# Optimization experiments

Measured on AMD Instinct MI355X. Metric: run time of the kernel, lower is better.

Reference implementation:

```python
import jax, jax.numpy as jnp
import numpy as np

HEADS = 16
S = 1024      # affine_dim
B, L = 4, 2048


def _conv1x1(x, W, b):
    # Conv1d with kernel_size=1: pointwise channel mixing. x: (B, C, L)
    return jnp.einsum('oc,bcl->bol', W, x) + b[None, :, None]


def setup_inputs() -> dict:
    key = jax.random.key(0)
    ks = jax.random.split(key, 7)
    scale = 1.0 / np.sqrt(S)  # ~ torch Conv1d default init scale
    return {
        'x':  jax.random.normal(ks[0], (B, S, L), dtype=jnp.float32),
        'Wk': jax.random.normal(ks[1], (S, S), dtype=jnp.float32) * scale,
        'bk': jax.random.normal(ks[2], (S,), dtype=jnp.float32) * scale,
        'Wq': jax.random.normal(ks[3], (S, S), dtype=jnp.float32) * scale,
        'bq': jax.random.normal(ks[4], (S,), dtype=jnp.float32) * scale,
        'Wp': jax.random.normal(ks[5], (S, S), dtype=jnp.float32) * scale,
        'bp': jax.random.normal(ks[6], (S,), dtype=jnp.float32) * scale,
    }


def reference(x, Wk, bk, Wq, bq, Wp, bp):
    b, c, l = x.shape
    h = HEADS
    d = c // h
    keys = _conv1x1(x, Wk, bk).reshape(b, h, d, l)
    queries = _conv1x1(x, Wq, bq).reshape(b, h, d, l)
    # scores[b,h,i,j] = sum_d keys[...,d,i] * queries[...,d,j]  (keys^T @ queries)
    # NOTE: original scales by `seqlen ** 1 / 2` == seqlen / 2 (Python precedence),
    # i.e. multiply by 2/L, NOT 1/sqrt(L). Faithfully preserved.
    scores = jnp.einsum('bhdi,bhdj->bhij', keys, queries) * (2.0 / l)
    attn = jax.nn.softmax(scores, axis=-1)
    xh = x.reshape(b, h, d, l)  # raw x used as values
    out = jnp.einsum('bhdi,bhij->bhdj', xh, attn).reshape(b, c, l)
    return _conv1x1(out, Wp, bp)
```

## Files before the change

kernel.cpp:

```cpp
#include <hip/hip_runtime.h>
#include <hip/hip_bf16.h>
#include <cstdint>
#include <cstddef>

#ifndef __has_builtin
#define __has_builtin(x) 0
#endif

#define DEVI __device__ __forceinline__

typedef __attribute__((ext_vector_type(8))) __bf16 bf16x8;
typedef __attribute__((ext_vector_type(4))) float float4v;
typedef __attribute__((ext_vector_type(16))) float float16v;
typedef __attribute__((ext_vector_type(4))) unsigned short ushort4v;
typedef __attribute__((ext_vector_type(4))) unsigned int uint4v;

constexpr int Bd = 4, Sd = 1024, Ld = 2048, Hd = 16, Dd = 64;

DEVI unsigned short f2bf(float x){
  union { float f; unsigned u; } v; v.f = x;
  unsigned r = v.u + 0x7fffu + ((v.u >> 16) & 1u);
  return (unsigned short)(r >> 16);
}

DEVI unsigned pack2(float lo, float hi){
  union { float f; unsigned u; } a, b; a.f = lo; b.f = hi;
  unsigned ra = a.u + 0x7fffu + ((a.u >> 16) & 1u);
  unsigned rb = b.u + 0x7fffu + ((b.u >> 16) & 1u);
#if __has_builtin(__builtin_amdgcn_perm)
  return __builtin_amdgcn_perm(rb, ra, 0x07060302u);
#else
  return (ra >> 16) | (rb & 0xffff0000u);
#endif
}

DEVI float fast_exp2(float x){
#if __has_builtin(__builtin_amdgcn_exp2f)
  return __builtin_amdgcn_exp2f(x);
#else
  return exp2f(x);
#endif
}

DEVI void plane32_swap(unsigned &a, unsigned &b){
  asm("v_permlane32_swap_b32 %0, %1" : "+v"(a), "+v"(b));
}

DEVI void gload_lds16(const void* g, void* lds){
  __builtin_amdgcn_global_load_lds(
      (const __attribute__((address_space(1))) void*)g,
      (__attribute__((address_space(3))) void*)lds,
      16, 0, 0);
}

DEVI float4v mfma_bf16(bf16x8 a, bf16x8 b, float4v c){
  return __builtin_amdgcn_mfma_f32_16x16x32_bf16(a, b, c, 0, 0, 0);
}

DEVI float16v mfma32_bf16(bf16x8 a, bf16x8 b, float16v c){
  return __builtin_amdgcn_mfma_f32_32x32x16_bf16(a, b, c, 0, 0, 0);
}


__global__ void wcast_kernel(const float* __restrict__ Wk, const float* __restrict__ Wq,
                             const float* __restrict__ Wp,
                             unsigned short* __restrict__ Wkbf, unsigned short* __restrict__ Wqbf,
                             unsigned short* __restrict__ Wpbf, float ck){
  size_t i = ((size_t)blockIdx.x * 256 + threadIdx.x) * 4;
  float4v a = *(const float4v*)(Wk + i);
  float4v b = *(const float4v*)(Wq + i);
  float4v c = *(const float4v*)(Wp + i);
  ushort4v oa = { f2bf(a[0]*ck), f2bf(a[1]*ck), f2bf(a[2]*ck), f2bf(a[3]*ck) };
  ushort4v ob = { f2bf(b[0]), f2bf(b[1]), f2bf(b[2]), f2bf(b[3]) };
  ushort4v oc = { f2bf(c[0]), f2bf(c[1]), f2bf(c[2]), f2bf(c[3]) };
  *(ushort4v*)(Wkbf + i) = oa;
  *(ushort4v*)(Wqbf + i) = ob;
  *(ushort4v*)(Wpbf + i) = oc;
}

__global__ void transpose_cast(const float* __restrict__ x, unsigned short* __restrict__ Xt){
  __shared__ float tile[32][33];
  const int b = blockIdx.z;
  const int l0 = blockIdx.x * 32;
  const int s0 = blockIdx.y * 32;
  const int tx = threadIdx.x, ty = threadIdx.y;
  #pragma unroll
  for (int r = 0; r < 32; r += 8)
    tile[ty + r][tx] = x[((size_t)b*Sd + s0 + ty + r)*Ld + l0 + tx];
  __syncthreads();
  #pragma unroll
  for (int r = 0; r < 32; r += 8)
    Xt[((size_t)b*Ld + l0 + ty + r)*Sd + s0 + tx] = f2bf(tile[tx][ty + r]);
}

__global__ void vprime_kernel(const float* __restrict__ x, const float* __restrict__ invZ,
                              unsigned short* __restrict__ Vp){
  size_t idx = ((size_t)blockIdx.x * 256 + threadIdx.x) * 4;
  const int l = (int)(idx & (Ld - 1));
  const int c = (int)((idx >> 11) & (Sd - 1));
  const int b = (int)(idx >> 21);
  const int h = c >> 6;
  float4v xv = *(const float4v*)(x + idx);
  float4v zv = *(const float4v*)(invZ + ((size_t)(b*Hd + h) * Ld + l));
  ushort4v o = { f2bf(xv[0]*zv[0]), f2bf(xv[1]*zv[1]), f2bf(xv[2]*zv[2]), f2bf(xv[3]*zv[3]) };
  *(ushort4v*)(Vp + idx) = o;
}

template<int OUT_MODE>
__global__ __launch_bounds__(256, 2)
void conv_gemm(const unsigned short* __restrict__ A,
               const unsigned short* __restrict__ Bt,
               const float* __restrict__ bias, float bscale,
               unsigned short* __restrict__ outT,
               float* __restrict__ outF)
{
  constexpr int BK = 32;
  constexpr int NKSTEP = Sd / BK;
  __shared__ __attribute__((aligned(16))) unsigned short Abuf[2][128*BK];
  __shared__ __attribute__((aligned(16))) unsigned short Bbuf[2][128*BK];

  const int b  = blockIdx.z;
  const int n0 = blockIdx.x * 128;
  const int m0 = blockIdx.y * 128;
  const int tid = threadIdx.x;
  const int w = tid >> 6, lane = tid & 63, lr = lane & 15, lg = lane >> 4;
  const int wm = (w >> 1) * 64, wn = (w & 1) * 64;

  const unsigned short* Abase = A + (size_t)m0 * Sd;
  const unsigned short* Bbase = Bt + ((size_t)b * Ld + n0) * Sd;

  auto stage = [&](int bf, int kt){
    #pragma unroll
    for (int p = 0; p < 2; ++p){
      int slot = p*256 + tid;
      int row = slot >> 2, c = slot & 3;
      int csrc = c ^ ((row >> 1) & 3);
      gload_lds16(Abase + (size_t)row * Sd + kt*BK + csrc*8,
                  (void*)(&Abuf[bf][(size_t)(p*256 + w*64) * 8]));
    }
    #pragma unroll
    for (int p = 0; p < 2; ++p){
      int slot = p*256 + tid;
      int row = slot >> 2, c = slot & 3;
      int csrc = c ^ ((row >> 1) & 3);
      gload_lds16(Bbase + (size_t)row * Sd + kt*BK + csrc*8,
                  (void*)(&Bbuf[bf][(size_t)(p*256 + w*64) * 8]));
    }
  };

  const int gsw = lg ^ ((lr >> 1) & 3);

  float4v acc[4][4];
  #pragma unroll
  for (int i = 0; i < 4; ++i)
    #pragma unroll
    for (int j = 0; j < 4; ++j)
      acc[i][j] = (float4v){0.f, 0.f, 0.f, 0.f};

  stage(0, 0);
  __syncthreads();
  int cur = 0;
  for (int kt = 0; kt < NKSTEP; ++kt){
    if (kt + 1 < NKSTEP) stage(cur ^ 1, kt + 1);
    bf16x8 af[4], bfv[4];
    #pragma unroll
    for (int i = 0; i < 4; ++i){
      int row = wm + i*16 + lr;
      af[i] = *(const bf16x8*)((const char*)&Abuf[cur][0] + (size_t)row*64 + gsw*16);
    }
    #pragma unroll
    for (int j = 0; j < 4; ++j){
      int row = wn + j*16 + lr;
      bfv[j] = *(const bf16x8*)((const char*)&Bbuf[cur][0] + (size_t)row*64 + gsw*16);
    }
    #pragma unroll
    for (int i = 0; i < 4; ++i)
      #pragma unroll
      for (int j = 0; j < 4; ++j)
        acc[i][j] = mfma_bf16(af[i], bfv[j], acc[i][j]);
    __syncthreads();
    cur ^= 1;
  }

  #pragma unroll
  for (int i = 0; i < 4; ++i){
    const int mb = m0 + wm + i*16 + lg*4;
    float4v bv = *(const float4v*)(bias + mb);
    #pragma unroll
    for (int j = 0; j < 4; ++j){
      const int n = n0 + wn + j*16 + lr;
      float4v v = acc[i][j];
      float o0 = v[0] + bscale*bv[0];
      float o1 = v[1] + bscale*bv[1];
      float o2 = v[2] + bscale*bv[2];
      float o3 = v[3] + bscale*bv[3];
      if (OUT_MODE == 0){
        ushort4v o = { f2bf(o0), f2bf(o1), f2bf(o2), f2bf(o3) };
        *(ushort4v*)(outT + ((size_t)b*Ld + n)*Sd + mb) = o;
      } else {
        outF[((size_t)b*Sd + mb + 0)*Ld + n] = o0;
        outF[((size_t)b*Sd + mb + 1)*Ld + n] = o1;
        outF[((size_t)b*Sd + mb + 2)*Ld + n] = o2;
        outF[((size_t)b*Sd + mb + 3)*Ld + n] = o3;
      }
    }
  }
}

__global__ __launch_bounds__(256, 4)
void stats_kernel(const unsigned short* __restrict__ Kt,
                  const unsigned short* __restrict__ Qt,
                  float* __restrict__ invZ)
{
  __shared__ __attribute__((aligned(16))) unsigned short Qbuf[2][64*64];

  const int m = blockIdx.x;
  const int xcd = m & 7, slot = m >> 3;
  const int bh = xcd * 8 + (slot >> 4);
  const int ib = slot & 15;
  const int b = bh >> 4, h = bh & 15;
  const int i0 = ib * 128;

  const int tid = threadIdx.x, w = tid >> 6, lane = tid & 63;
  const int l31 = lane & 31, lh = lane >> 5;
  const int iw = i0 + w * 32;

  bf16x8 kb[4];
  #pragma unroll
  for (int ks = 0; ks < 4; ++ks)
    kb[ks] = *(const bf16x8*)(Kt + ((size_t)b*Ld + iw + l31)*Sd + h*64 + ks*16 + lh*8);

  const size_t qbase = (size_t)b*Ld*Sd + (size_t)h*64;
  auto stage = [&](int bf, int jt){
    const int j0 = jt * 64;
    #pragma unroll
    for (int p = 0; p < 2; ++p){
      const int slot2 = p*256 + tid;
      const int row = slot2 >> 3;
      const int gsrc = (slot2 & 7) ^ (row & 7);
      gload_lds16(Qt + qbase + (size_t)(j0 + row)*Sd + gsrc*8,
                  (void*)(&Qbuf[bf][(size_t)slot2 * 8]));
    }
  };

  float z = 0.f;
  stage(0, 0);
  __syncthreads();
  int cur = 0;
  for (int jt = 0; jt < 32; ++jt){
    if (jt + 1 < 32) stage(cur ^ 1, jt + 1);
    #pragma unroll
    for (int js = 0; js < 2; ++js){
      float16v sacc;
      #pragma unroll
      for (int r = 0; r < 16; ++r) sacc[r] = 0.f;
      #pragma unroll
      for (int ks = 0; ks < 4; ++ks){
        const int row = js*32 + l31;
        const int g = (2*ks + lh) ^ (l31 & 7);
        bf16x8 qf = *(const bf16x8*)((const char*)&Qbuf[cur][0] + (size_t)row*128 + g*16);
        sacc = mfma32_bf16(qf, kb[ks], sacc);
      }
      #pragma unroll
      for (int r = 0; r < 16; ++r) z += fast_exp2(sacc[r]);
    }
    __syncthreads();
    cur ^= 1;
  }

  z += __shfl_xor(z, 32, 64);
  if (lh == 0)
    invZ[(size_t)bh * Ld + iw + l31] = 1.0f / z;
}

__global__ __launch_bounds__(256, 4)
void attn_pv_kernel(const unsigned short* __restrict__ Kt,
                    const unsigned short* __restrict__ Qt,
                    const unsigned short* __restrict__ Vp,
                    unsigned short* __restrict__ AOt)
{
  __shared__ __attribute__((aligned(16))) unsigned short Kbuf[2][64*64];
  __shared__ __attribute__((aligned(16))) unsigned short Vbuf[2][64*64];

  const int m = blockIdx.x;
  const int xcd = m & 7, slot = m >> 3;
  const int bh = xcd * 8 + (slot >> 4);
  const int jb = slot & 15;
  const int b = bh >> 4, h = bh & 15;
  const int j0 = jb * 128;

  const int tid = threadIdx.x, w = tid >> 6, lane = tid & 63;
  const int l31 = lane & 31, lh = lane >> 5;
  const int jw = j0 + w * 32;

  bf16x8 qb[4];
  #pragma unroll
  for (int ks = 0; ks < 4; ++ks)
    qb[ks] = *(const bf16x8*)(Qt + ((size_t)b*Ld + jw + l31)*Sd + h*64 + ks*16 + lh*8);

  float16v oacc[2];
  #pragma unroll
  for (int ds = 0; ds < 2; ++ds)
    #pragma unroll
    for (int r = 0; r < 16; ++r) oacc[ds][r] = 0.f;

  const size_t kbase = (size_t)b*Ld*Sd + (size_t)h*64;
  const size_t vbase = ((size_t)b*Sd + h*64)*Ld;

  auto stage = [&](int bf, int it){
    const int i0 = it * 64;
    #pragma unroll
    for (int p = 0; p < 2; ++p){
      const int slot2 = p*256 + tid;
      const int row = slot2 >> 3;
      const int gsrc = (slot2 & 7) ^ (row & 7);
      gload_lds16(Kt + kbase + (size_t)(i0 + row)*Sd + gsrc*8,
                  (void*)(&Kbuf[bf][(size_t)slot2 * 8]));
      gload_lds16(Vp + vbase + (size_t)row*Ld + i0 + gsrc*8,
                  (void*)(&Vbuf[bf][(size_t)slot2 * 8]));
    }
  };

  stage(0, 0);
  __syncthreads();
  int cur = 0;
  for (int it = 0; it < 32; ++it){
    if (it + 1 < 32) stage(cur ^ 1, it + 1);

    float16v sacc[2];
    #pragma unroll
    for (int is = 0; is < 2; ++is){
      #pragma unroll
      for (int r = 0; r < 16; ++r) sacc[is][r] = 0.f;
      #pragma unroll
      for (int ks = 0; ks < 4; ++ks){
        const int row = is*32 + l31;
        const int g = (2*ks + lh) ^ (l31 & 7);
        bf16x8 kf = *(const bf16x8*)((const char*)&Kbuf[cur][0] + (size_t)row*128 + g*16);
        sacc[is] = mfma32_bf16(kf, qb[ks], sacc[is]);
      }
    }

    bf16x8 pf[4];
    #pragma unroll
    for (int is = 0; is < 2; ++is){
      #pragma unroll
      for (int hs = 0; hs < 2; ++hs){
        const int r0 = 8*hs;
        unsigned W0 = pack2(fast_exp2(sacc[is][r0+0]), fast_exp2(sacc[is][r0+1]));
        unsigned W1 = pack2(fast_exp2(sacc[is][r0+2]), fast_exp2(sacc[is][r0+3]));
        unsigned W2 = pack2(fast_exp2(sacc[is][r0+4]), fast_exp2(sacc[is][r0+5]));
        unsigned W3 = pack2(fast_exp2(sacc[is][r0+6]), fast_exp2(sacc[is][r0+7]));
        plane32_swap(W0, W2);
        plane32_swap(W1, W3);
        union { uint4v u; bf16x8 v; } cvt;
        cvt.u = (uint4v){ W0, W1, W2, W3 };
        pf[is*2 + hs] = cvt.v;
      }
    }

    #pragma unroll
    for (int kp = 0; kp < 4; ++kp){
      #pragma unroll
      for (int ds = 0; ds < 2; ++ds){
        const int row = ds*32 + l31;
        const int g = (2*kp + lh) ^ (l31 & 7);
        bf16x8 vf = *(const bf16x8*)((const char*)&Vbuf[cur][0] + (size_t)row*128 + g*16);
        oacc[ds] = mfma32_bf16(vf, pf[kp], oacc[ds]);
      }
    }

    __syncthreads();
    cur ^= 1;
  }

  #pragma unroll
  for (int ds = 0; ds < 2; ++ds){
    #pragma unroll
    for (int rq = 0; rq < 4; ++rq){
      const int d0 = ds*32 + 8*rq + 4*lh;
      ushort4v o = { f2bf(oacc[ds][4*rq+0]), f2bf(oacc[ds][4*rq+1]),
                     f2bf(oacc[ds][4*rq+2]), f2bf(oacc[ds][4*rq+3]) };
      *(ushort4v*)(AOt + ((size_t)b*Ld + jw + l31)*Sd + h*64 + d0) = o;
    }
  }
}


extern "C" void kernel_launch(void* const* d_in, const int* in_sizes, int n_in,
                              void* d_out, int out_size, void* d_ws, size_t ws_size,
                              hipStream_t stream)
{
  const float* x  = (const float*)d_in[0];
  const float* Wk = (const float*)d_in[1];
  const float* bk = (const float*)d_in[2];
  const float* Wq = (const float*)d_in[3];
  const float* bq = (const float*)d_in[4];
  const float* Wp = (const float*)d_in[5];
  const float* bp = (const float*)d_in[6];
  float* out = (float*)d_out;

  char* ws = (char*)d_ws;
  const size_t SZ_BLS = (size_t)Bd * Ld * Sd * 2;
  unsigned short* Xt   = (unsigned short*)(ws);
  unsigned short* Kt   = (unsigned short*)(ws + SZ_BLS);
  unsigned short* Qt   = (unsigned short*)(ws + 2*SZ_BLS);
  unsigned short* AOt  = (unsigned short*)(ws + 3*SZ_BLS);
  unsigned short* Wkbf = (unsigned short*)(ws + 4*SZ_BLS);
  unsigned short* Wqbf = (unsigned short*)(ws + 4*SZ_BLS + (size_t)2097152);
  unsigned short* Wpbf = (unsigned short*)(ws + 4*SZ_BLS + (size_t)2*2097152);
  float* invZ          = (float*)(ws + 4*SZ_BLS + (size_t)3*2097152);
  unsigned short* Vp   = Xt;

  const float ck = (2.0f / (float)Ld) * 1.44269504088896f;

  wcast_kernel<<<1024, 256, 0, stream>>>(Wk, Wq, Wp, Wkbf, Wqbf, Wpbf, ck);
  transpose_cast<<<dim3(Ld/32, Sd/32, Bd), dim3(32, 8), 0, stream>>>(x, Xt);

  dim3 cg(Ld/128, Sd/128, Bd);
  conv_gemm<0><<<cg, 256, 0, stream>>>(Wkbf, Xt, bk, ck,   Kt, nullptr);
  conv_gemm<0><<<cg, 256, 0, stream>>>(Wqbf, Xt, bq, 1.0f, Qt, nullptr);

  stats_kernel<<<dim3((Ld/128)*(Bd*Hd)), 256, 0, stream>>>(Kt, Qt, invZ);
  vprime_kernel<<<(Bd*(size_t)Sd*Ld/4)/256, 256, 0, stream>>>(x, invZ, Vp);
  attn_pv_kernel<<<dim3((Ld/128)*(Bd*Hd)), 256, 0, stream>>>(Kt, Qt, Vp, AOt);

  conv_gemm<1><<<cg, 256, 0, stream>>>(Wpbf, AOt, bp, 1.0f, nullptr, out);
}
```

Before: 235.6 us.

## Double per-wave tile in stats and attention kernels, add MFMA priority hints

Each wave in the stats and attn_pv kernels now owns 64 rows or columns instead of 32, so each LDS-staged K/Q/V tile is reused across two MFMA sub-tiles and the grid is halved. K and V fragments are loaded into registers once per iteration, and s_setprio brackets the MFMA runs. The P-to-bf16 pack switches from round-to-nearest-even to a simpler round-half-up add. The larger tiles raise register use, so launch bounds for attn_pv drop to 2 blocks per CU, trading occupancy for reuse. The grid shrinks to 512 blocks.

```diff
diff --git a/kernel.cpp b/kernel.cpp
--- a/kernel.cpp
+++ b/kernel.cpp
@@ -25,8 +25,8 @@
 
 DEVI unsigned pack2(float lo, float hi){
   union { float f; unsigned u; } a, b; a.f = lo; b.f = hi;
-  unsigned ra = a.u + 0x7fffu + ((a.u >> 16) & 1u);
-  unsigned rb = b.u + 0x7fffu + ((b.u >> 16) & 1u);
+  unsigned ra = a.u + 0x8000u;
+  unsigned rb = b.u + 0x8000u;
 #if __has_builtin(__builtin_amdgcn_perm)
   return __builtin_amdgcn_perm(rb, ra, 0x07060302u);
 #else
@@ -216,19 +216,21 @@
 
   const int m = blockIdx.x;
   const int xcd = m & 7, slot = m >> 3;
-  const int bh = xcd * 8 + (slot >> 4);
-  const int ib = slot & 15;
+  const int bh = xcd * 8 + (slot >> 3);
+  const int ib = slot & 7;
   const int b = bh >> 4, h = bh & 15;
-  const int i0 = ib * 128;
+  const int i0 = ib * 256;
 
   const int tid = threadIdx.x, w = tid >> 6, lane = tid & 63;
   const int l31 = lane & 31, lh = lane >> 5;
-  const int iw = i0 + w * 32;
-
-  bf16x8 kb[4];
-  #pragma unroll
-  for (int ks = 0; ks < 4; ++ks)
-    kb[ks] = *(const bf16x8*)(Kt + ((size_t)b*Ld + iw + l31)*Sd + h*64 + ks*16 + lh*8);
+  const int iw0 = i0 + w * 64;
+
+  bf16x8 kb[2][4];
+  #pragma unroll
+  for (int is = 0; is < 2; ++is)
+    #pragma unroll
+    for (int ks = 0; ks < 4; ++ks)
+      kb[is][ks] = *(const bf16x8*)(Kt + ((size_t)b*Ld + iw0 + is*32 + l31)*Sd + h*64 + ks*16 + lh*8);
 
   const size_t qbase = (size_t)b*Ld*Sd + (size_t)h*64;
   auto stage = [&](int bf, int jt){
@@ -243,7 +245,7 @@
     }
   };
 
-  float z = 0.f;
+  float z[2] = {0.f, 0.f};
   stage(0, 0);
   __syncthreads();
   int cur = 0;
@@ -251,29 +253,40 @@
     if (jt + 1 < 32) stage(cur ^ 1, jt + 1);
     #pragma unroll
     for (int js = 0; js < 2; ++js){
-      float16v sacc;
-      #pragma unroll
-      for (int r = 0; r < 16; ++r) sacc[r] = 0.f;
+      bf16x8 qf[4];
       #pragma unroll
       for (int ks = 0; ks < 4; ++ks){
         const int row = js*32 + l31;
         const int g = (2*ks + lh) ^ (l31 & 7);
-        bf16x8 qf = *(const bf16x8*)((const char*)&Qbuf[cur][0] + (size_t)row*128 + g*16);
-        sacc = mfma32_bf16(qf, kb[ks], sacc);
-      }
-      #pragma unroll
-      for (int r = 0; r < 16; ++r) z += fast_exp2(sacc[r]);
+        qf[ks] = *(const bf16x8*)((const char*)&Qbuf[cur][0] + (size_t)row*128 + g*16);
+      }
+      #pragma unroll
+      for (int is = 0; is < 2; ++is){
+        float16v sacc;
+        #pragma unroll
+        for (int r = 0; r < 16; ++r) sacc[r] = 0.f;
+        __builtin_amdgcn_s_setprio(1);
+        #pragma unroll
+        for (int ks = 0; ks < 4; ++ks)
+          sacc = mfma32_bf16(qf[ks], kb[is][ks], sacc);
+        __builtin_amdgcn_s_setprio(0);
+        #pragma unroll
+        for (int r = 0; r < 16; ++r) z[is] += fast_exp2(sacc[r]);
+      }
     }
     __syncthreads();
     cur ^= 1;
   }
 
-  z += __shfl_xor(z, 32, 64);
-  if (lh == 0)
-    invZ[(size_t)bh * Ld + iw + l31] = 1.0f / z;
-}
-
-__global__ __launch_bounds__(256, 4)
+  #pragma unroll
+  for (int is = 0; is < 2; ++is){
+    float zv = z[is] + __shfl_xor(z[is], 32, 64);
+    if (lh == 0)
+      invZ[(size_t)bh * Ld + iw0 + is*32 + l31] = 1.0f / zv;
+  }
+}
+
+__global__ __launch_bounds__(256, 2)
 void attn_pv_kernel(const unsigned short* __restrict__ Kt,
                     const unsigned short* __restrict__ Qt,
                     const unsigned short* __restrict__ Vp,
@@ -284,25 +297,29 @@
 
   const int m = blockIdx.x;
   const int xcd = m & 7, slot = m >> 3;
-  const int bh = xcd * 8 + (slot >> 4);
-  const int jb = slot & 15;
+  const int bh = xcd * 8 + (slot >> 3);
+  const int jb = slot & 7;
   const int b = bh >> 4, h = bh & 15;
-  const int j0 = jb * 128;
+  const int j0 = jb * 256;
 
   const int tid = threadIdx.x, w = tid >> 6, lane = tid & 63;
   const int l31 = lane & 31, lh = lane >> 5;
-  const int jw = j0 + w * 32;
-
-  bf16x8 qb[4];
-  #pragma unroll
-  for (int ks = 0; ks < 4; ++ks)
-    qb[ks] = *(const bf16x8*)(Qt + ((size_t)b*Ld + jw + l31)*Sd + h*64 + ks*16 + lh*8);
-
-  float16v oacc[2];
+  const int jw = j0 + w * 64;
+
+  bf16x8 qb[2][4];
+  #pragma unroll
+  for (int js = 0; js < 2; ++js)
+    #pragma unroll
+    for (int ks = 0; ks < 4; ++ks)
+      qb[js][ks] = *(const bf16x8*)(Qt + ((size_t)b*Ld + jw + js*32 + l31)*Sd + h*64 + ks*16 + lh*8);
+
+  float16v oacc[2][2];
   #pragma unroll
   for (int ds = 0; ds < 2; ++ds)
     #pragma unroll
-    for (int r = 0; r < 16; ++r) oacc[ds][r] = 0.f;
+    for (int js = 0; js < 2; ++js)
+      #pragma unroll
+      for (int r = 0; r < 16; ++r) oacc[ds][js][r] = 0.f;
 
   const size_t kbase = (size_t)b*Ld*Sd + (size_t)h*64;
   const size_t vbase = ((size_t)b*Sd + h*64)*Ld;
@@ -327,47 +344,58 @@
   for (int it = 0; it < 32; ++it){
     if (it + 1 < 32) stage(cur ^ 1, it + 1);
 
-    float16v sacc[2];
-    #pragma unroll
-    for (int is = 0; is < 2; ++is){
-      #pragma unroll
-      for (int r = 0; r < 16; ++r) sacc[is][r] = 0.f;
+    bf16x8 kf[2][4], vf[2][4];
+    #pragma unroll
+    for (int is = 0; is < 2; ++is)
       #pragma unroll
       for (int ks = 0; ks < 4; ++ks){
         const int row = is*32 + l31;
         const int g = (2*ks + lh) ^ (l31 & 7);
-        bf16x8 kf = *(const bf16x8*)((const char*)&Kbuf[cur][0] + (size_t)row*128 + g*16);
-        sacc[is] = mfma32_bf16(kf, qb[ks], sacc[is]);
-      }
-    }
-
-    bf16x8 pf[4];
-    #pragma unroll
-    for (int is = 0; is < 2; ++is){
-      #pragma unroll
-      for (int hs = 0; hs < 2; ++hs){
-        const int r0 = 8*hs;
-        unsigned W0 = pack2(fast_exp2(sacc[is][r0+0]), fast_exp2(sacc[is][r0+1]));
-        unsigned W1 = pack2(fast_exp2(sacc[is][r0+2]), fast_exp2(sacc[is][r0+3]));
-        unsigned W2 = pack2(fast_exp2(sacc[is][r0+4]), fast_exp2(sacc[is][r0+5]));
-        unsigned W3 = pack2(fast_exp2(sacc[is][r0+6]), fast_exp2(sacc[is][r0+7]));
-        plane32_swap(W0, W2);
-        plane32_swap(W1, W3);
-        union { uint4v u; bf16x8 v; } cvt;
-        cvt.u = (uint4v){ W0, W1, W2, W3 };
-        pf[is*2 + hs] = cvt.v;
-      }
-    }
-
-    #pragma unroll
-    for (int kp = 0; kp < 4; ++kp){
-      #pragma unroll
-      for (int ds = 0; ds < 2; ++ds){
-        const int row = ds*32 + l31;
-        const int g = (2*kp + lh) ^ (l31 & 7);
-        bf16x8 vf = *(const bf16x8*)((const char*)&Vbuf[cur][0] + (size_t)row*128 + g*16);
-        oacc[ds] = mfma32_bf16(vf, pf[kp], oacc[ds]);
-      }
+        kf[is][ks] = *(const bf16x8*)((const char*)&Kbuf[cur][0] + (size_t)row*128 + g*16);
+        vf[is][ks] = *(const bf16x8*)((const char*)&Vbuf[cur][0] + (size_t)row*128 + g*16);
+      }
+
+    #pragma unroll
+    for (int js = 0; js < 2; ++js){
+      float16v sacc[2];
+      #pragma unroll
+      for (int is = 0; is < 2; ++is){
+        #pragma unroll
+        for (int r = 0; r < 16; ++r) sacc[is][r] = 0.f;
+      }
+      __builtin_amdgcn_s_setprio(1);
+      #pragma unroll
+      for (int is = 0; is < 2; ++is)
+        #pragma unroll
+        for (int ks = 0; ks < 4; ++ks)
+          sacc[is] = mfma32_bf16(kf[is][ks], qb[js][ks], sacc[is]);
+      __builtin_amdgcn_s_setprio(0);
+
+      bf16x8 pf[4];
+      #pragma unroll
+      for (int is = 0; is < 2; ++is){
+        #pragma unroll
+        for (int hs = 0; hs < 2; ++hs){
+          const int r0 = 8*hs;
+          unsigned W0 = pack2(fast_exp2(sacc[is][r0+0]), fast_exp2(sacc[is][r0+1]));
+          unsigned W1 = pack2(fast_exp2(sacc[is][r0+2]), fast_exp2(sacc[is][r0+3]));
+          unsigned W2 = pack2(fast_exp2(sacc[is][r0+4]), fast_exp2(sacc[is][r0+5]));
+          unsigned W3 = pack2(fast_exp2(sacc[is][r0+6]), fast_exp2(sacc[is][r0+7]));
+          plane32_swap(W0, W2);
+          plane32_swap(W1, W3);
+          union { uint4v u; bf16x8 v; } cvt;
+          cvt.u = (uint4v){ W0, W1, W2, W3 };
+          pf[is*2 + hs] = cvt.v;
+        }
+      }
+
+      __builtin_amdgcn_s_setprio(1);
+      #pragma unroll
+      for (int kp = 0; kp < 4; ++kp)
+        #pragma unroll
+        for (int ds = 0; ds < 2; ++ds)
+          oacc[ds][js] = mfma32_bf16(vf[ds][kp], pf[kp], oacc[ds][js]);
+      __builtin_amdgcn_s_setprio(0);
     }
 
     __syncthreads();
@@ -375,15 +403,16 @@
   }
 
   #pragma unroll
-  for (int ds = 0; ds < 2; ++ds){
-    #pragma unroll
-    for (int rq = 0; rq < 4; ++rq){
-      const int d0 = ds*32 + 8*rq + 4*lh;
-      ushort4v o = { f2bf(oacc[ds][4*rq+0]), f2bf(oacc[ds][4*rq+1]),
-                     f2bf(oacc[ds][4*rq+2]), f2bf(oacc[ds][4*rq+3]) };
-      *(ushort4v*)(AOt + ((size_t)b*Ld + jw + l31)*Sd + h*64 + d0) = o;
-    }
-  }
+  for (int ds = 0; ds < 2; ++ds)
+    #pragma unroll
+    for (int js = 0; js < 2; ++js)
+      #pragma unroll
+      for (int rq = 0; rq < 4; ++rq){
+        const int d0 = ds*32 + 8*rq + 4*lh;
+        ushort4v o = { f2bf(oacc[ds][js][4*rq+0]), f2bf(oacc[ds][js][4*rq+1]),
+                       f2bf(oacc[ds][js][4*rq+2]), f2bf(oacc[ds][js][4*rq+3]) };
+        *(ushort4v*)(AOt + ((size_t)b*Ld + jw + js*32 + l31)*Sd + h*64 + d0) = o;
+      }
 }
 
 
@@ -421,9 +450,9 @@
   conv_gemm<0><<<cg, 256, 0, stream>>>(Wkbf, Xt, bk, ck,   Kt, nullptr);
   conv_gemm<0><<<cg, 256, 0, stream>>>(Wqbf, Xt, bq, 1.0f, Qt, nullptr);
 
-  stats_kernel<<<dim3((Ld/128)*(Bd*Hd)), 256, 0, stream>>>(Kt, Qt, invZ);
+  stats_kernel<<<dim3((Ld/256)*(Bd*Hd)), 256, 0, stream>>>(Kt, Qt, invZ);
   vprime_kernel<<<(Bd*(size_t)Sd*Ld/4)/256, 256, 0, stream>>>(x, invZ, Vp);
-  attn_pv_kernel<<<dim3((Ld/128)*(Bd*Hd)), 256, 0, stream>>>(Kt, Qt, Vp, AOt);
+  attn_pv_kernel<<<dim3((Ld/256)*(Bd*Hd)), 256, 0, stream>>>(Kt, Qt, Vp, AOt);
 
   conv_gemm<1><<<cg, 256, 0, stream>>>(Wpbf, AOt, bp, 1.0f, nullptr, out);
 }
```

Result: faster. 227.5 us (-3.4%).
